# Optimization experiments

Hardware: AMD Instinct MI355X
Metric: run time of the kernel (lower is better)

Reference implementation:

```python
import jax, jax.numpy as jnp
import numpy as np

NB = 8      # number of diagonal blocks per layer
BIN = 512   # in-block size
BOUT = 512  # out-block size


def setup_inputs() -> dict:
    key = jax.random.key(0)
    k_x, k_w1, k_b1, k_w2, k_b2 = jax.random.split(key, 5)
    B, D = 8192, NB * BIN
    x = jax.random.normal(k_x, (B, D), dtype=jnp.float32)
    # Block-diagonal weights stored as stacked blocks [NB, out_blk, in_blk]
    s1 = 1.0 / np.sqrt(BIN)
    W1 = jax.random.uniform(k_w1, (NB, BOUT, BIN), jnp.float32, -s1, s1)
    b1 = jax.random.uniform(k_b1, (NB * BOUT,), jnp.float32, -s1, s1)
    s2 = 1.0 / np.sqrt(BIN)
    W2 = jax.random.uniform(k_w2, (NB, BOUT, BIN), jnp.float32, -s2, s2)
    b2 = jax.random.uniform(k_b2, (NB * BOUT,), jnp.float32, -s2, s2)
    return {"x": x, "W1": W1, "b1": b1, "W2": W2, "b2": b2}


def _blockdiag_linear(x, W, b):
    # x: [B, NB*BIN]; W: [NB, BOUT, BIN]; b: [NB*BOUT]
    B = x.shape[0]
    xb = x.reshape(B, NB, BIN)                      # [B, NB, BIN]
    yb = jnp.einsum('bnc,noc->bno', xb, W)          # block-diag matmul
    return yb.reshape(B, NB * W.shape[1]) + b


def reference(x, W1, b1, W2, b2):
    x = x.reshape(x.shape[0], -1)                   # flatten(start_dim=1)
    h = jax.nn.relu(_blockdiag_linear(x, W1, b1))
    out = jax.nn.relu(_blockdiag_linear(h, W2, b2))
    return out
```

## Files before the change

### kernel.cpp

```cpp
#include <hip/hip_runtime.h>
#include <hip/hip_bf16.h>

#define NB 8
#define BIN 512
#define BOUT 512
#define BATCH 8192
#define DIM 4096

typedef __attribute__((ext_vector_type(8))) short bf16x8;
typedef __attribute__((ext_vector_type(4))) float f32x4;

#define SWZ(r) (((r) & 7) << 4)

__device__ __forceinline__ unsigned short f2bf_rne(float f) {
    unsigned u = __builtin_bit_cast(unsigned, f);
    unsigned r = (u + 0x7FFFu + ((u >> 16) & 1u)) >> 16;
    return (unsigned short)r;
}

__device__ __forceinline__ unsigned long long pack4(f32x4 f) {
    return (unsigned long long)f2bf_rne(f.x)
         | ((unsigned long long)f2bf_rne(f.y) << 16)
         | ((unsigned long long)f2bf_rne(f.z) << 32)
         | ((unsigned long long)f2bf_rne(f.w) << 48);
}

__global__ void pack_w(const float* __restrict__ W, unsigned short* __restrict__ pk) {
    int gid = blockIdx.x * 256 + threadIdx.x;
    int lane = gid & 63;
    int n    = (gid >> 6) & 7;
    int kidx = (gid >> 9) & 15;
    int wn   = (gid >> 13) & 3;
    int nb   = gid >> 15;
    int row  = wn * 128 + n * 16 + (lane & 15);
    int col  = kidx * 32 + (lane >> 4) * 8;
    const float* s = W + ((size_t)nb * BOUT + row) * BIN + col;
    f32x4 a = *(const f32x4*)s;
    f32x4 b = *(const f32x4*)(s + 4);
    unsigned long long* d = (unsigned long long*)(pk + (size_t)gid * 8);
    d[0] = pack4(a);
    d[1] = pack4(b);
}

__global__ __launch_bounds__(256, 2)
void fused_mlp(const float* __restrict__ X,
               const unsigned short* __restrict__ PK1,
               const float* __restrict__ B1,
               const unsigned short* __restrict__ PK2,
               const float* __restrict__ B2,
               float* __restrict__ Out)
{
    __shared__ __align__(16) unsigned char pool[65536];
    unsigned char* As = pool;
    unsigned char* Hs = pool;

    const int bid = blockIdx.x;
    const int nb = bid & 7;
    const int mt = bid >> 3;

    const int t = threadIdx.x;
    const int lane = t & 63;
    const int wn = t >> 6;
    const int l15 = lane & 15;
    const int lhi = lane >> 4;

    const int row0 = mt * 64;
    const int wc0  = nb * 512;

    const int sr = t >> 2;
    const int sc = (t & 3) * 16;

    const unsigned short* s1 = PK1 + (size_t)(nb * 4 + wn) * 65536;
    const unsigned short* s2 = PK2 + (size_t)(nb * 4 + wn) * 65536;

    f32x4 acc[4][8];
    #pragma unroll
    for (int m = 0; m < 4; m++)
        #pragma unroll
        for (int n = 0; n < 8; n++)
            acc[m][n] = (f32x4)(0.f);

    f32x4 xp[4];
    bf16x8 q0[8], q1[8];

#define LOAD_XP(KT) { \
    _Pragma("unroll") for (int j = 0; j < 4; j++) \
        xp[j] = *(const f32x4*)(X + (size_t)(row0 + sr) * DIM + wc0 + (KT) * 64 + sc + j * 4); }

#define STAGE_AS(BUF) { \
    _Pragma("unroll") for (int h2 = 0; h2 < 2; h2++) { \
        bf16x8 v; \
        ((unsigned long long*)&v)[0] = pack4(xp[h2 * 2 + 0]); \
        ((unsigned long long*)&v)[1] = pack4(xp[h2 * 2 + 1]); \
        *(bf16x8*)(As + (BUF) * 8192 + sr * 128 + (((sc + 8 * h2) * 2) ^ SWZ(sr))) = v; } }

#define LOADQ(Q, S, KIDX) { \
    _Pragma("unroll") for (int n = 0; n < 8; n++) \
        Q[n] = *(const bf16x8*)((S) + ((KIDX) * 8 + n) * 512 + lane * 8); }

#define MFMA32(Q, AF) \
    __builtin_amdgcn_s_setprio(1); \
    _Pragma("unroll") for (int m = 0; m < 4; m++) \
        _Pragma("unroll") for (int n = 0; n < 8; n++) \
            acc[m][n] = __builtin_amdgcn_mfma_f32_16x16x32_bf16(AF[m], Q[n], acc[m][n], 0, 0, 0); \
    __builtin_amdgcn_s_setprio(0);

#define P1STEP(Q, BUF, KS) { \
    bf16x8 af[4]; \
    const int cb_ = ((KS) * 32 + lhi * 8) * 2; \
    _Pragma("unroll") for (int m = 0; m < 4; m++) { \
        const int r_ = m * 16 + l15; \
        af[m] = *(const bf16x8*)(As + (BUF) * 8192 + r_ * 128 + (cb_ ^ SWZ(r_))); } \
    MFMA32(Q, af) }

#define P2STEP(Q, KIDX) { \
    bf16x8 af[4]; \
    const int cb_ = ((KIDX) * 32 + lhi * 8) * 2; \
    _Pragma("unroll") for (int m = 0; m < 4; m++) { \
        const int r_ = m * 16 + l15; \
        af[m] = *(const bf16x8*)(Hs + r_ * 1024 + (cb_ ^ SWZ(r_))); } \
    MFMA32(Q, af) }

#define BAR() { \
    asm volatile("s_waitcnt lgkmcnt(0)" ::: "memory"); \
    __builtin_amdgcn_s_barrier(); \
    __builtin_amdgcn_sched_barrier(0); }

    LOAD_XP(0);
    STAGE_AS(0);
    LOAD_XP(1);
    LOADQ(q0, s1, 0);
    BAR();

    #pragma unroll
    for (int kt = 0; kt < 8; kt++) {
        const int buf = kt & 1;
        LOADQ(q1, s1, 2 * kt + 1);
        P1STEP(q0, buf, 0);
        if (kt < 7) { STAGE_AS(buf ^ 1); }
        if (kt < 6) { LOAD_XP(kt + 2); }
        if (kt < 7) { LOADQ(q0, s1, 2 * kt + 2); }
        else        { LOADQ(q0, s2, 0); }
        P1STEP(q1, buf, 1);
        BAR();
    }

    #pragma unroll
    for (int n = 0; n < 8; n++) {
        const int c = wn * 128 + n * 16 + l15;
        const float bv = B1[wc0 + c];
        #pragma unroll
        for (int m = 0; m < 4; m++) {
            #pragma unroll
            for (int rr = 0; rr < 4; rr++) {
                float v = acc[m][n][rr] + bv;
                v = v > 0.f ? v : 0.f;
                const int r = m * 16 + lhi * 4 + rr;
                *(unsigned short*)(Hs + r * 1024 + ((c * 2) ^ SWZ(r))) = f2bf_rne(v);
            }
        }
    }
    BAR();

    #pragma unroll
    for (int m = 0; m < 4; m++)
        #pragma unroll
        for (int n = 0; n < 8; n++)
            acc[m][n] = (f32x4)(0.f);

    #pragma unroll
    for (int kk = 0; kk < 8; kk++) {
        LOADQ(q1, s2, 2 * kk + 1);
        P2STEP(q0, 2 * kk);
        if (kk < 7) { LOADQ(q0, s2, 2 * kk + 2); }
        P2STEP(q1, 2 * kk + 1);
    }

    #pragma unroll
    for (int n = 0; n < 8; n++) {
        const int c = wc0 + wn * 128 + n * 16 + l15;
        const float bv = B2[c];
        #pragma unroll
        for (int m = 0; m < 4; m++) {
            const int rb = row0 + m * 16 + lhi * 4;
            #pragma unroll
            for (int rr = 0; rr < 4; rr++) {
                float v = acc[m][n][rr] + bv;
                Out[(size_t)(rb + rr) * DIM + c] = v > 0.f ? v : 0.f;
            }
        }
    }

#undef LOAD_XP
#undef STAGE_AS
#undef LOADQ
#undef MFMA32
#undef P1STEP
#undef P2STEP
#undef BAR
}

extern "C" void kernel_launch(void* const* d_in, const int* in_sizes, int n_in,
                              void* d_out, int out_size, void* d_ws, size_t ws_size,
                              hipStream_t stream) {
    const float* x  = (const float*)d_in[0];
    const float* W1 = (const float*)d_in[1];
    const float* b1 = (const float*)d_in[2];
    const float* W2 = (const float*)d_in[3];
    const float* b2 = (const float*)d_in[4];
    float* out = (float*)d_out;

    char* ws = (char*)d_ws;
    unsigned short* PK1 = (unsigned short*)ws;
    unsigned short* PK2 = (unsigned short*)(ws + (4u << 20));

    pack_w<<<1024, 256, 0, stream>>>(W1, PK1);
    pack_w<<<1024, 256, 0, stream>>>(W2, PK2);

    const int GRID = NB * (BATCH / 64);
    fused_mlp<<<GRID, 256, 0, stream>>>(x, PK1, b1, PK2, b2, out);
}
```

Baseline: 105.7 us.

## Stage full X tile into LDS upfront, remove per-k-tile barriers in layer one

Loads and converts the whole 64x512 X slice to bf16 in LDS once at the start, then runs layer one with no barriers, the same way layer two runs. This removes the eight per-iteration barriers and the double-buffered staging of X that was interleaved with the MFMAs. In exchange, the global loads of X are no longer overlapped with compute: all of them must finish before the first MFMA, which exposes that load latency.

```diff
diff --git a/kernel.cpp b/kernel.cpp
--- a/kernel.cpp
+++ b/kernel.cpp
@@ -50,9 +50,7 @@
                const float* __restrict__ B2,
                float* __restrict__ Out)
 {
-    __shared__ __align__(16) unsigned char pool[65536];
-    unsigned char* As = pool;
-    unsigned char* Hs = pool;
+    __shared__ __align__(16) unsigned char LB[65536];
 
     const int bid = blockIdx.x;
     const int nb = bid & 7;
@@ -67,9 +65,6 @@
     const int row0 = mt * 64;
     const int wc0  = nb * 512;
 
-    const int sr = t >> 2;
-    const int sc = (t & 3) * 16;
-
     const unsigned short* s1 = PK1 + (size_t)(nb * 4 + wn) * 65536;
     const unsigned short* s2 = PK2 + (size_t)(nb * 4 + wn) * 65536;
 
@@ -80,19 +75,7 @@
         for (int n = 0; n < 8; n++)
             acc[m][n] = (f32x4)(0.f);
 
-    f32x4 xp[4];
     bf16x8 q0[8], q1[8];
-
-#define LOAD_XP(KT) { \
-    _Pragma("unroll") for (int j = 0; j < 4; j++) \
-        xp[j] = *(const f32x4*)(X + (size_t)(row0 + sr) * DIM + wc0 + (KT) * 64 + sc + j * 4); }
-
-#define STAGE_AS(BUF) { \
-    _Pragma("unroll") for (int h2 = 0; h2 < 2; h2++) { \
-        bf16x8 v; \
-        ((unsigned long long*)&v)[0] = pack4(xp[h2 * 2 + 0]); \
-        ((unsigned long long*)&v)[1] = pack4(xp[h2 * 2 + 1]); \
-        *(bf16x8*)(As + (BUF) * 8192 + sr * 128 + (((sc + 8 * h2) * 2) ^ SWZ(sr))) = v; } }
 
 #define LOADQ(Q, S, KIDX) { \
     _Pragma("unroll") for (int n = 0; n < 8; n++) \
@@ -105,45 +88,59 @@
             acc[m][n] = __builtin_amdgcn_mfma_f32_16x16x32_bf16(AF[m], Q[n], acc[m][n], 0, 0, 0); \
     __builtin_amdgcn_s_setprio(0);
 
-#define P1STEP(Q, BUF, KS) { \
+#define HALFSTEP(QCUR, QNXT, SNXT, KNXT, KIDX) { \
+    LOADQ(QNXT, SNXT, KNXT); \
     bf16x8 af[4]; \
-    const int cb_ = ((KS) * 32 + lhi * 8) * 2; \
+    const int cb_ = (KIDX) * 64 + lhi * 16; \
     _Pragma("unroll") for (int m = 0; m < 4; m++) { \
         const int r_ = m * 16 + l15; \
-        af[m] = *(const bf16x8*)(As + (BUF) * 8192 + r_ * 128 + (cb_ ^ SWZ(r_))); } \
-    MFMA32(Q, af) }
-
-#define P2STEP(Q, KIDX) { \
+        af[m] = *(const bf16x8*)(LB + r_ * 1024 + (cb_ ^ SWZ(r_))); } \
+    MFMA32(QCUR, af) }
+
+#define HALFSTEP_NL(QCUR, KIDX) { \
     bf16x8 af[4]; \
-    const int cb_ = ((KIDX) * 32 + lhi * 8) * 2; \
+    const int cb_ = (KIDX) * 64 + lhi * 16; \
     _Pragma("unroll") for (int m = 0; m < 4; m++) { \
         const int r_ = m * 16 + l15; \
-        af[m] = *(const bf16x8*)(Hs + r_ * 1024 + (cb_ ^ SWZ(r_))); } \
-    MFMA32(Q, af) }
+        af[m] = *(const bf16x8*)(LB + r_ * 1024 + (cb_ ^ SWZ(r_))); } \
+    MFMA32(QCUR, af) }
 
 #define BAR() { \
     asm volatile("s_waitcnt lgkmcnt(0)" ::: "memory"); \
     __builtin_amdgcn_s_barrier(); \
     __builtin_amdgcn_sched_barrier(0); }
 
-    LOAD_XP(0);
-    STAGE_AS(0);
-    LOAD_XP(1);
     LOADQ(q0, s1, 0);
+
+    {
+        const int sr = t >> 2;
+        const float* xr = X + (size_t)(row0 + sr) * DIM + wc0 + (t & 3) * 128;
+        const int j0 = (t & 3) * 16;
+        #pragma unroll
+        for (int i = 0; i < 8; i++) {
+            f32x4 a = *(const f32x4*)(xr + i * 16 + 0);
+            f32x4 b = *(const f32x4*)(xr + i * 16 + 4);
+            f32x4 c = *(const f32x4*)(xr + i * 16 + 8);
+            f32x4 d = *(const f32x4*)(xr + i * 16 + 12);
+            bf16x8 v0, v1;
+            ((unsigned long long*)&v0)[0] = pack4(a);
+            ((unsigned long long*)&v0)[1] = pack4(b);
+            ((unsigned long long*)&v1)[0] = pack4(c);
+            ((unsigned long long*)&v1)[1] = pack4(d);
+            *(bf16x8*)(LB + sr * 1024 + (((j0 + 2 * i)     * 16) ^ SWZ(sr))) = v0;
+            *(bf16x8*)(LB + sr * 1024 + (((j0 + 2 * i + 1) * 16) ^ SWZ(sr))) = v1;
+        }
+    }
     BAR();
 
     #pragma unroll
-    for (int kt = 0; kt < 8; kt++) {
-        const int buf = kt & 1;
-        LOADQ(q1, s1, 2 * kt + 1);
-        P1STEP(q0, buf, 0);
-        if (kt < 7) { STAGE_AS(buf ^ 1); }
-        if (kt < 6) { LOAD_XP(kt + 2); }
-        if (kt < 7) { LOADQ(q0, s1, 2 * kt + 2); }
-        else        { LOADQ(q0, s2, 0); }
-        P1STEP(q1, buf, 1);
-        BAR();
-    }
+    for (int kp = 0; kp < 8; kp++) {
+        HALFSTEP(q0, q1, s1, 2 * kp + 1, 2 * kp);
+        if (kp < 7) { HALFSTEP(q1, q0, s1, 2 * kp + 2, 2 * kp + 1) }
+        else        { HALFSTEP(q1, q0, s2, 0,          15)         }
+    }
+
+    BAR();
 
     #pragma unroll
     for (int n = 0; n < 8; n++) {
@@ -156,7 +153,7 @@
                 float v = acc[m][n][rr] + bv;
                 v = v > 0.f ? v : 0.f;
                 const int r = m * 16 + lhi * 4 + rr;
-                *(unsigned short*)(Hs + r * 1024 + ((c * 2) ^ SWZ(r))) = f2bf_rne(v);
+                *(unsigned short*)(LB + r * 1024 + ((c * 2) ^ SWZ(r))) = f2bf_rne(v);
             }
         }
     }
@@ -169,11 +166,10 @@
             acc[m][n] = (f32x4)(0.f);
 
     #pragma unroll
-    for (int kk = 0; kk < 8; kk++) {
-        LOADQ(q1, s2, 2 * kk + 1);
-        P2STEP(q0, 2 * kk);
-        if (kk < 7) { LOADQ(q0, s2, 2 * kk + 2); }
-        P2STEP(q1, 2 * kk + 1);
+    for (int kp = 0; kp < 8; kp++) {
+        HALFSTEP(q0, q1, s2, 2 * kp + 1, 2 * kp);
+        if (kp < 7) { HALFSTEP(q1, q0, s2, 2 * kp + 2, 2 * kp + 1) }
+        else        { HALFSTEP_NL(q1, 15) }
     }
 
     #pragma unroll
@@ -191,12 +187,10 @@
         }
     }
 
-#undef LOAD_XP
-#undef STAGE_AS
 #undef LOADQ
 #undef MFMA32
-#undef P1STEP
-#undef P2STEP
+#undef HALFSTEP
+#undef HALFSTEP_NL
 #undef BAR
 }
 
```

Measured after the change: 104.9 us. About the same (-0.8%).
